# Performance work log

Hardware: AMD Instinct MI355X
Metric: run time of the kernel (lower is better)

The kernel has to match this reference:

```python
import jax, jax.numpy as jnp
import numpy as np

EMBED = 1024
HEADS = 16
HEAD_DIM = EMBED // HEADS


def setup_inputs() -> dict:
    key = jax.random.key(0)
    ks = jax.random.split(key, 8)
    b, t, d = 2, 2048, EMBED
    s = 1.0 / np.sqrt(d)
    return {
        'k': jax.random.normal(ks[0], (b, t, d), jnp.float32),
        'q': jax.random.normal(ks[1], (b, t, d), jnp.float32),
        'v': jax.random.normal(ks[2], (b, t, d), jnp.float32),
        'Wk': jax.random.normal(ks[3], (d, d), jnp.float32) * s,
        'Wq': jax.random.normal(ks[4], (d, d), jnp.float32) * s,
        'Wv': jax.random.normal(ks[5], (d, d), jnp.float32) * s,
        'Wo': jax.random.normal(ks[6], (d, d), jnp.float32) * s,
        'bo': jax.random.normal(ks[7], (d,), jnp.float32) * 0.01,
    }


def reference(k, q, v, Wk, Wq, Wv, Wo, bo):
    b, t, d = q.shape
    h, n = HEADS, HEAD_DIM
    # projections (q_prj bias=False, k/v bias=False per add_bias_kv=False)
    keys = (k @ Wk.T).reshape(b, t, h, n).transpose(0, 2, 1, 3)      # b h t n
    queries = (q @ Wq.T).reshape(b, t, h, n).transpose(0, 2, 1, 3)
    values = (v @ Wv.T).reshape(b, t, h, n).transpose(0, 2, 1, 3)
    att = jnp.einsum('bhtn,bhsn->bhts', queries, keys)               # b h t t
    att = jax.nn.softmax(att / np.sqrt(n), axis=-1)
    out = jnp.einsum('bhts,bhsn->bhtn', att, values)                 # b h t n
    out = out.transpose(0, 2, 1, 3).reshape(b, t, d)                 # b t (h n)
    return out @ Wo.T + bo
```

## Files before the change

kernel.cpp:

```cpp
#include <hip/hip_runtime.h>
#include <hip/hip_bf16.h>


typedef unsigned short u16;
typedef unsigned int   u32;
using short8 = __attribute__((ext_vector_type(8))) short;
using f32x4  = __attribute__((ext_vector_type(4))) float;

__device__ __forceinline__ u16 f2b(float f) {
    u32 u = __float_as_uint(f);
    u += 0x7FFFu + ((u >> 16) & 1u);
    return (u16)(u >> 16);
}
__device__ __forceinline__ u32 pack2(float lo, float hi) {
    union { __hip_bfloat162 h; u32 u; } c;
    c.h = __float22bfloat162_rn(make_float2(lo, hi));
    return c.u;
}
__device__ __forceinline__ void gld_lds16(const u16* g, u16* l) {
    __builtin_amdgcn_global_load_lds(
        (const __attribute__((address_space(1))) void*)g,
        (__attribute__((address_space(3))) void*)l, 16, 0, 0);
}

__global__ __launch_bounds__(256) void convert_kernel(
    const float* s0, const float* s1, const float* s2, const float* s3,
    const float* s4, const float* s5, const float* s6,
    u16* d0, u16* d1, u16* d2, u16* d3, u16* d4, u16* d5, u16* d6)
{
    const int y = blockIdx.y;
    const float* s; u16* d; u32 n;
    switch (y) {
        case 0: s = s0; d = d0; n = 1048576; break;
        case 1: s = s1; d = d1; n = 1048576; break;
        case 2: s = s2; d = d2; n = 1048576; break;
        case 3: s = s3; d = d3; n = 262144; break;
        case 4: s = s4; d = d4; n = 262144; break;
        case 5: s = s5; d = d5; n = 262144; break;
        default: s = s6; d = d6; n = 262144; break;
    }
    for (u32 i = blockIdx.x * 256 + threadIdx.x; i < n; i += 256 * 1024) {
        float4 f = ((const float4*)s)[i];
        uint2 o; o.x = pack2(f.x, f.y); o.y = pack2(f.z, f.w);
        ((uint2*)d)[i] = o;
    }
}

template <int MODE>
__device__ __forceinline__ void gemm_core(
    const u16* __restrict__ A, const u16* __restrict__ B,
    void* __restrict__ C, const float* __restrict__ bias, float scale,
    u32 bm, u32 bn)
{
    constexpr u32 K = 1024;
    __shared__ u16 As[128 * 32];
    __shared__ u16 Bs[128 * 32];

    const int tid  = threadIdx.x;
    const int lane = tid & 63;
    const int w    = tid >> 6;
    const int wr   = w >> 1, wc = w & 1;
    const int ml   = lane & 15, g = lane >> 4;

    f32x4 acc[4][4] = {};

    const u32 srow = w * 32 + (lane >> 2);
    const u32 scol = (u32)(((lane & 3) ^ ((lane >> 3) & 3)) * 8);
    const u16* gA = A + (size_t)(bm + srow) * K + scol;
    const u16* gB = B + (size_t)(bn + srow) * K + scol;
    u16* lA = &As[w * 1024];
    u16* lB = &Bs[w * 1024];

    const u32 fsw = (u32)((g ^ ((ml >> 1) & 3)) * 8);

    for (u32 k0 = 0; k0 < K; k0 += 32) {
        __syncthreads();
        gld_lds16(gA + k0, lA);
        gld_lds16(gA + 16 * K + k0, lA + 512);
        gld_lds16(gB + k0, lB);
        gld_lds16(gB + 16 * K + k0, lB + 512);
        __syncthreads();

        short8 af[4], bf[4];
#pragma unroll
        for (int it = 0; it < 4; ++it)
            af[it] = *(const short8*)&As[(wr * 64 + it * 16 + ml) * 32 + fsw];
#pragma unroll
        for (int ct = 0; ct < 4; ++ct)
            bf[ct] = *(const short8*)&Bs[(wc * 64 + ct * 16 + ml) * 32 + fsw];
#pragma unroll
        for (int it = 0; it < 4; ++it)
#pragma unroll
            for (int ct = 0; ct < 4; ++ct)
                acc[it][ct] = __builtin_amdgcn_mfma_f32_16x16x32_bf16(
                    af[it], bf[ct], acc[it][ct], 0, 0, 0);
    }

    if (MODE == 3) {
#pragma unroll
        for (int ct = 0; ct < 4; ++ct) {
            const u32 col = bn + wc * 64 + ct * 16 + ml;
            u16* dst = (u16*)C + (col >> 11) * 2097152 + (col & 2047);
#pragma unroll
            for (int it = 0; it < 4; ++it) {
                const u32 row = bm + wr * 64 + it * 16 + g * 4;
#pragma unroll
                for (int r = 0; r < 4; ++r)
                    dst[(size_t)(row + r) * 2048] = f2b(acc[it][ct][r]);
            }
        }
    } else {
#pragma unroll
        for (int ct = 0; ct < 4; ++ct) {
            const u32 col = bn + wc * 64 + ct * 16 + ml;
            const float bv = (MODE == 2 && bias) ? bias[col] : 0.0f;
#pragma unroll
            for (int it = 0; it < 4; ++it) {
                const u32 row = bm + wr * 64 + it * 16 + g * 4;
#pragma unroll
                for (int r = 0; r < 4; ++r) {
                    const float v = acc[it][ct][r] * scale + bv;
                    if (MODE == 2) ((float*)C)[(size_t)(row + r) * 1024 + col] = v;
                    else           ((u16*)C)[(size_t)(row + r) * 1024 + col] = f2b(v);
                }
            }
        }
    }
}

__global__ __launch_bounds__(256) void proj3_kernel(
    const u16* kb, const u16* qb, const u16* vb,
    const u16* Wkb, const u16* Wqb, const u16* Wvb,
    u16* Kp, u16* Qp, u16* Vt)
{
    if (blockIdx.z == 0)
        gemm_core<0>(kb, Wkb, Kp, nullptr, 1.0f, blockIdx.y * 128, blockIdx.x * 128);
    else if (blockIdx.z == 1)
        gemm_core<0>(qb, Wqb, Qp, nullptr, 0.18033688011112042f, blockIdx.y * 128, blockIdx.x * 128);
    else
        gemm_core<3>(Wvb, vb, Vt, nullptr, 1.0f, blockIdx.x * 128, blockIdx.y * 128);
}

__global__ __launch_bounds__(256) void out_gemm_kernel(
    const u16* A, const u16* W, float* C, const float* bias)
{
    gemm_core<2>(A, W, C, bias, 1.0f, blockIdx.y * 128, blockIdx.x * 128);
}

__global__ __launch_bounds__(256) void attn_kernel(
    const u16* __restrict__ Qp, const u16* __restrict__ Kp,
    const u16* __restrict__ Vt, u16* __restrict__ Op)
{
    __shared__ u16   Ps[4 * 2048];
    __shared__ float R0[4096];
    __shared__ float Lr[256];

    const int tid  = threadIdx.x;
    const int lane = tid & 63;
    const int w    = tid >> 6;
    const int ml   = lane & 15;
    const int g    = lane >> 4;
    const u32 bh   = blockIdx.y;
    const u32 b    = bh >> 4, h = bh & 15;
    const u32 t0   = blockIdx.x * 64;

    const u32 base  = b * 2048 * 1024 + h * 64;
    const u32 vbase = bh * 64 * 2048;

    short8 bq[4][2];
#pragma unroll
    for (int qt = 0; qt < 4; ++qt) {
        const u16* qr = Qp + base + (t0 + qt * 16 + ml) * 1024 + g * 8;
        bq[qt][0] = *(const short8*)qr;
        bq[qt][1] = *(const short8*)(qr + 32);
    }

    f32x4 oacc[4][4] = {};
    float l4[4] = {};

    u16* Pw = &Ps[w * 2048];
    u32* Pw32 = (u32*)Pw;

    u32 kOff = base + (w * 32 + ml) * 1024 + g * 8;
    u32 vOff = vbase + ml * 2048 + w * 32 + g * 8;

    for (int it = 0; it < 16; ++it) {
        short8 va[4];
#pragma unroll
        for (int dt = 0; dt < 4; ++dt)
            va[dt] = *(const short8*)(Vt + vOff + dt * 16 * 2048);

#pragma unroll
        for (int sub = 0; sub < 2; ++sub) {
            const u16* kp = Kp + kOff + sub * 16 * 1024;
            short8 ka0 = *(const short8*)kp;
            short8 ka1 = *(const short8*)(kp + 32);
            const u32 ch = (u32)(sub * 2 + (g >> 1));
#pragma unroll
            for (int qt = 0; qt < 4; ++qt) {
                f32x4 z = {};
                z = __builtin_amdgcn_mfma_f32_16x16x32_bf16(ka0, bq[qt][0], z, 0, 0, 0);
                z = __builtin_amdgcn_mfma_f32_16x16x32_bf16(ka1, bq[qt][1], z, 0, 0, 0);
                const float p0 = exp2f(z[0]), p1 = exp2f(z[1]);
                const float p2 = exp2f(z[2]), p3 = exp2f(z[3]);
                l4[qt] += (p0 + p1) + (p2 + p3);
                const u32 q = (u32)(qt * 16 + ml);
                const u32 idx = q * 16 + ((ch ^ ((q >> 1) & 3)) << 2) + (g & 1) * 2;
                uint2 pv; pv.x = pack2(p0, p1); pv.y = pack2(p2, p3);
                *(uint2*)&Pw32[idx] = pv;
            }
        }
        kOff += 128 * 1024;
        vOff += 128;

        short8 pb[4];
#pragma unroll
        for (int qt = 0; qt < 4; ++qt) {
            const u32 q = (u32)(qt * 16 + ml);
            pb[qt] = *(const short8*)&Pw[q * 32 + ((g ^ ((q >> 1) & 3)) * 8)];
        }
#pragma unroll
        for (int dt = 0; dt < 4; ++dt)
#pragma unroll
            for (int qt = 0; qt < 4; ++qt)
                oacc[dt][qt] = __builtin_amdgcn_mfma_f32_16x16x32_bf16(
                    va[dt], pb[qt], oacc[dt][qt], 0, 0, 0);
    }

#pragma unroll
    for (int qt = 0; qt < 4; ++qt) {
        l4[qt] += __shfl_xor(l4[qt], 16);
        l4[qt] += __shfl_xor(l4[qt], 32);
    }
    if (g == 0) {
#pragma unroll
        for (int qt = 0; qt < 4; ++qt) Lr[w * 64 + qt * 16 + ml] = l4[qt];
    }
    __syncthreads();
    float* R1 = (float*)Ps;

#define WRITE_R(Rp)                                                          \
    {_Pragma("unroll") for (int dt = 0; dt < 4; ++dt)                        \
     _Pragma("unroll") for (int qt = 0; qt < 4; ++qt)                        \
     _Pragma("unroll") for (int r = 0; r < 4; ++r)                           \
        (Rp)[(dt * 16 + g * 4 + r) * 64 + qt * 16 + ml] = oacc[dt][qt][r];}
#define ADD_R(Rp)                                                            \
    {_Pragma("unroll") for (int dt = 0; dt < 4; ++dt)                        \
     _Pragma("unroll") for (int qt = 0; qt < 4; ++qt)                        \
     _Pragma("unroll") for (int r = 0; r < 4; ++r)                           \
        oacc[dt][qt][r] += (Rp)[(dt * 16 + g * 4 + r) * 64 + qt * 16 + ml];}

    if (w == 1) WRITE_R(R0)
    if (w == 3) WRITE_R(R1)
    __syncthreads();
    if (w == 0) ADD_R(R0)
    if (w == 2) ADD_R(R1)
    __syncthreads();
    if (w == 2) WRITE_R(R0)
    __syncthreads();
    if (w == 0) {
        ADD_R(R0)
#pragma unroll
        for (int qt = 0; qt < 4; ++qt) {
            const u32 q = (u32)(qt * 16 + ml);
            const float inv = 1.0f / (Lr[q] + Lr[64 + q] + Lr[128 + q] + Lr[192 + q]);
            const u32 row = (b * 2048 + t0 + q) * 1024 + h * 64;
#pragma unroll
            for (int dt = 0; dt < 4; ++dt) {
                const u32 ci = row + dt * 16 + g * 4;
                *(u32*)&Op[ci]     = pack2(oacc[dt][qt][0] * inv, oacc[dt][qt][1] * inv);
                *(u32*)&Op[ci + 2] = pack2(oacc[dt][qt][2] * inv, oacc[dt][qt][3] * inv);
            }
        }
    }
#undef WRITE_R
#undef ADD_R
}

extern "C" void kernel_launch(void* const* d_in, const int* in_sizes, int n_in,
                              void* d_out, int out_size, void* d_ws, size_t ws_size,
                              hipStream_t stream)
{
    const float* kin = (const float*)d_in[0];
    const float* qin = (const float*)d_in[1];
    const float* vin = (const float*)d_in[2];
    const float* Wk  = (const float*)d_in[3];
    const float* Wq  = (const float*)d_in[4];
    const float* Wv  = (const float*)d_in[5];
    const float* Wo  = (const float*)d_in[6];
    const float* bo  = (const float*)d_in[7];
    float* out = (float*)d_out;

    const size_t ACT = 4194304;
    const size_t WSZ = 1048576;

    u16* kb  = (u16*)d_ws;
    u16* qb  = kb + ACT;
    u16* vb  = qb + ACT;
    u16* Wkb = vb + ACT;
    u16* Wqb = Wkb + WSZ;
    u16* Wvb = Wqb + WSZ;
    u16* Wob = Wvb + WSZ;
    u16* Kp  = Wob + WSZ;
    u16* Qp  = Kp + ACT;
    u16* Vt  = Qp + ACT;
    u16* Op  = kb;

    convert_kernel<<<dim3(1024, 7), 256, 0, stream>>>(
        kin, qin, vin, Wk, Wq, Wv, Wo, kb, qb, vb, Wkb, Wqb, Wvb, Wob);
    proj3_kernel<<<dim3(8, 32, 3), 256, 0, stream>>>(
        kb, qb, vb, Wkb, Wqb, Wvb, Kp, Qp, Vt);
    attn_kernel<<<dim3(32, 32), 256, 0, stream>>>(Qp, Kp, Vt, Op);
    out_gemm_kernel<<<dim3(8, 32), 256, 0, stream>>>(Op, Wob, out, bo);
}
```

Before: 245.9 us.

## Double-buffer K/V loads in attention, use fast exp2, retile output GEMM

The attention loop now prefetches the next K and V register tiles while the current step computes, which aims to hide global load latency. It also switches exp2f to the hardware exp2 intrinsic and adds a launch-bounds occupancy hint of 2. The output projection gets its own 64x128-tile GEMM, launched with twice as many blocks, to improve CU utilisation. The costs are higher register pressure, which may conflict with the occupancy hint, and slightly less accurate exponentials.

```diff
diff --git a/kernel.cpp b/kernel.cpp
--- a/kernel.cpp
+++ b/kernel.cpp
@@ -16,6 +16,9 @@
     union { __hip_bfloat162 h; u32 u; } c;
     c.h = __float22bfloat162_rn(make_float2(lo, hi));
     return c.u;
+}
+__device__ __forceinline__ float fexp2(float x) {
+    return __builtin_amdgcn_exp2f(x);
 }
 __device__ __forceinline__ void gld_lds16(const u16* g, u16* l) {
     __builtin_amdgcn_global_load_lds(
@@ -142,12 +145,67 @@
 }
 
 __global__ __launch_bounds__(256) void out_gemm_kernel(
-    const u16* A, const u16* W, float* C, const float* bias)
-{
-    gemm_core<2>(A, W, C, bias, 1.0f, blockIdx.y * 128, blockIdx.x * 128);
-}
-
-__global__ __launch_bounds__(256) void attn_kernel(
+    const u16* __restrict__ A, const u16* __restrict__ W,
+    float* __restrict__ C, const float* __restrict__ bias)
+{
+    constexpr u32 K = 1024;
+    __shared__ u16 As[64 * 32];
+    __shared__ u16 Bs[128 * 32];
+
+    const int tid  = threadIdx.x;
+    const int lane = tid & 63;
+    const int w    = tid >> 6;
+    const int wr   = w >> 1, wc = w & 1;
+    const int ml   = lane & 15, g = lane >> 4;
+    const u32 bm   = blockIdx.y * 64, bn = blockIdx.x * 128;
+
+    f32x4 acc[2][4] = {};
+
+    const u32 scol = (u32)(((lane & 3) ^ ((lane >> 3) & 3)) * 8);
+    const u16* gA = A + (size_t)(bm + w * 16 + (lane >> 2)) * K + scol;
+    const u16* gB = W + (size_t)(bn + w * 32 + (lane >> 2)) * K + scol;
+    u16* lA = &As[w * 512];
+    u16* lB = &Bs[w * 1024];
+
+    const u32 fsw = (u32)((g ^ ((ml >> 1) & 3)) * 8);
+
+    for (u32 k0 = 0; k0 < K; k0 += 32) {
+        __syncthreads();
+        gld_lds16(gA + k0, lA);
+        gld_lds16(gB + k0, lB);
+        gld_lds16(gB + 16 * K + k0, lB + 512);
+        __syncthreads();
+
+        short8 af[2], bf[4];
+#pragma unroll
+        for (int it = 0; it < 2; ++it)
+            af[it] = *(const short8*)&As[(wr * 32 + it * 16 + ml) * 32 + fsw];
+#pragma unroll
+        for (int ct = 0; ct < 4; ++ct)
+            bf[ct] = *(const short8*)&Bs[(wc * 64 + ct * 16 + ml) * 32 + fsw];
+#pragma unroll
+        for (int it = 0; it < 2; ++it)
+#pragma unroll
+            for (int ct = 0; ct < 4; ++ct)
+                acc[it][ct] = __builtin_amdgcn_mfma_f32_16x16x32_bf16(
+                    af[it], bf[ct], acc[it][ct], 0, 0, 0);
+    }
+
+#pragma unroll
+    for (int ct = 0; ct < 4; ++ct) {
+        const u32 col = bn + wc * 64 + ct * 16 + ml;
+        const float bv = bias ? bias[col] : 0.0f;
+#pragma unroll
+        for (int it = 0; it < 2; ++it) {
+            const u32 row = bm + wr * 32 + it * 16 + g * 4;
+#pragma unroll
+            for (int r = 0; r < 4; ++r)
+                C[(size_t)(row + r) * 1024 + col] = acc[it][ct][r] + bv;
+        }
+    }
+}
+
+__global__ __launch_bounds__(256, 2) void attn_kernel(
     const u16* __restrict__ Qp, const u16* __restrict__ Kp,
     const u16* __restrict__ Vt, u16* __restrict__ Op)
 {
@@ -184,48 +242,73 @@
     u32 kOff = base + (w * 32 + ml) * 1024 + g * 8;
     u32 vOff = vbase + ml * 2048 + w * 32 + g * 8;
 
-    for (int it = 0; it < 16; ++it) {
-        short8 va[4];
-#pragma unroll
-        for (int dt = 0; dt < 4; ++dt)
-            va[dt] = *(const short8*)(Vt + vOff + dt * 16 * 2048);
-
-#pragma unroll
-        for (int sub = 0; sub < 2; ++sub) {
-            const u16* kp = Kp + kOff + sub * 16 * 1024;
-            short8 ka0 = *(const short8*)kp;
-            short8 ka1 = *(const short8*)(kp + 32);
-            const u32 ch = (u32)(sub * 2 + (g >> 1));
-#pragma unroll
-            for (int qt = 0; qt < 4; ++qt) {
-                f32x4 z = {};
-                z = __builtin_amdgcn_mfma_f32_16x16x32_bf16(ka0, bq[qt][0], z, 0, 0, 0);
-                z = __builtin_amdgcn_mfma_f32_16x16x32_bf16(ka1, bq[qt][1], z, 0, 0, 0);
-                const float p0 = exp2f(z[0]), p1 = exp2f(z[1]);
-                const float p2 = exp2f(z[2]), p3 = exp2f(z[3]);
-                l4[qt] += (p0 + p1) + (p2 + p3);
-                const u32 q = (u32)(qt * 16 + ml);
-                const u32 idx = q * 16 + ((ch ^ ((q >> 1) & 3)) << 2) + (g & 1) * 2;
-                uint2 pv; pv.x = pack2(p0, p1); pv.y = pack2(p2, p3);
-                *(uint2*)&Pw32[idx] = pv;
-            }
-        }
-        kOff += 128 * 1024;
-        vOff += 128;
-
-        short8 pb[4];
-#pragma unroll
-        for (int qt = 0; qt < 4; ++qt) {
-            const u32 q = (u32)(qt * 16 + ml);
-            pb[qt] = *(const short8*)&Pw[q * 32 + ((g ^ ((q >> 1) & 3)) * 8)];
-        }
-#pragma unroll
-        for (int dt = 0; dt < 4; ++dt)
-#pragma unroll
-            for (int qt = 0; qt < 4; ++qt)
-                oacc[dt][qt] = __builtin_amdgcn_mfma_f32_16x16x32_bf16(
-                    va[dt], pb[qt], oacc[dt][qt], 0, 0, 0);
-    }
+    short8 va[2][4], ka[2][2][2];
+#pragma unroll
+    for (int dt = 0; dt < 4; ++dt)
+        va[0][dt] = *(const short8*)(Vt + vOff + dt * 32768);
+#pragma unroll
+    for (int sub = 0; sub < 2; ++sub) {
+        const u16* kp = Kp + kOff + sub * 16384;
+        ka[0][sub][0] = *(const short8*)kp;
+        ka[0][sub][1] = *(const short8*)(kp + 32);
+    }
+    kOff += 131072; vOff += 128;
+
+#define ATTN_STEP(CUR, NXT, PREF)                                            \
+    {                                                                        \
+        if (PREF) {                                                          \
+            _Pragma("unroll")                                                \
+            for (int dt = 0; dt < 4; ++dt)                                   \
+                va[NXT][dt] = *(const short8*)(Vt + vOff + dt * 32768);      \
+            _Pragma("unroll")                                                \
+            for (int sub = 0; sub < 2; ++sub) {                              \
+                const u16* kp = Kp + kOff + sub * 16384;                     \
+                ka[NXT][sub][0] = *(const short8*)kp;                        \
+                ka[NXT][sub][1] = *(const short8*)(kp + 32);                 \
+            }                                                                \
+            kOff += 131072; vOff += 128;                                     \
+        }                                                                    \
+        _Pragma("unroll")                                                    \
+        for (int sub = 0; sub < 2; ++sub) {                                  \
+            const u32 ch = (u32)(sub * 2 + (g >> 1));                        \
+            _Pragma("unroll")                                                \
+            for (int qt = 0; qt < 4; ++qt) {                                 \
+                f32x4 z = {};                                                \
+                z = __builtin_amdgcn_mfma_f32_16x16x32_bf16(                 \
+                    ka[CUR][sub][0], bq[qt][0], z, 0, 0, 0);                 \
+                z = __builtin_amdgcn_mfma_f32_16x16x32_bf16(                 \
+                    ka[CUR][sub][1], bq[qt][1], z, 0, 0, 0);                 \
+                const float p0 = fexp2(z[0]), p1 = fexp2(z[1]);              \
+                const float p2 = fexp2(z[2]), p3 = fexp2(z[3]);              \
+                l4[qt] += (p0 + p1) + (p2 + p3);                             \
+                const u32 q = (u32)(qt * 16 + ml);                           \
+                const u32 idx = q * 16 + ((ch ^ ((q >> 1) & 3)) << 2)        \
+                                + (g & 1) * 2;                               \
+                uint2 pv; pv.x = pack2(p0, p1); pv.y = pack2(p2, p3);        \
+                *(uint2*)&Pw32[idx] = pv;                                    \
+            }                                                                \
+        }                                                                    \
+        short8 pb[4];                                                        \
+        _Pragma("unroll")                                                    \
+        for (int qt = 0; qt < 4; ++qt) {                                     \
+            const u32 q = (u32)(qt * 16 + ml);                               \
+            pb[qt] = *(const short8*)&Pw[q * 32 + ((g ^ ((q >> 1) & 3)) * 8)]; \
+        }                                                                    \
+        _Pragma("unroll")                                                    \
+        for (int dt = 0; dt < 4; ++dt)                                       \
+            _Pragma("unroll")                                                \
+            for (int qt = 0; qt < 4; ++qt)                                   \
+                oacc[dt][qt] = __builtin_amdgcn_mfma_f32_16x16x32_bf16(      \
+                    va[CUR][dt], pb[qt], oacc[dt][qt], 0, 0, 0);             \
+    }
+
+    for (int it = 0; it < 7; ++it) {
+        ATTN_STEP(0, 1, true)
+        ATTN_STEP(1, 0, true)
+    }
+    ATTN_STEP(0, 1, true)
+    ATTN_STEP(1, 0, false)
+#undef ATTN_STEP
 
 #pragma unroll
     for (int qt = 0; qt < 4; ++qt) {
@@ -311,5 +394,5 @@
     proj3_kernel<<<dim3(8, 32, 3), 256, 0, stream>>>(
         kb, qb, vb, Wkb, Wqb, Wvb, Kp, Qp, Vt);
     attn_kernel<<<dim3(32, 32), 256, 0, stream>>>(Qp, Kp, Vt, Op);
-    out_gemm_kernel<<<dim3(8, 32), 256, 0, stream>>>(Op, Wob, out, bo);
-}
+    out_gemm_kernel<<<dim3(8, 64), 256, 0, stream>>>(Op, Wob, out, bo);
+}
```

New measurement: 229.6 us. 6.7% less time.
